# Kernel optimization log

Measured on AMD Instinct MI355X. Metric: run time of the kernel, lower is better.

Reference implementation:

```python
import jax, jax.numpy as jnp
import numpy as np
import math

D_MODEL = 2048
NUM_HEADS = 16
HEAD_DIM = D_MODEL // NUM_HEADS  # 128
B, S = 2, 2048


def setup_inputs() -> dict:
    key = jax.random.key(0)
    ks = jax.random.split(key, 11)
    s_in = 1.0 / math.sqrt(D_MODEL)
    return {
        "query": jax.random.normal(ks[0], (B, S, D_MODEL), dtype=jnp.float32),
        "key": jax.random.normal(ks[1], (B, S, D_MODEL), dtype=jnp.float32),
        "value": jax.random.normal(ks[2], (B, S, D_MODEL), dtype=jnp.float32),
        "Wq": jax.random.normal(ks[3], (D_MODEL, D_MODEL), dtype=jnp.float32) * s_in,
        "bq": jnp.zeros((D_MODEL,), dtype=jnp.float32),
        "Wk": jax.random.normal(ks[4], (D_MODEL, HEAD_DIM), dtype=jnp.float32) * s_in,
        "bk": jnp.zeros((HEAD_DIM,), dtype=jnp.float32),
        "Wv": jax.random.normal(ks[5], (D_MODEL, HEAD_DIM), dtype=jnp.float32) * s_in,
        "bv": jnp.zeros((HEAD_DIM,), dtype=jnp.float32),
        "Wo": jax.random.normal(ks[6], (D_MODEL, D_MODEL), dtype=jnp.float32) * s_in,
        "bo": jnp.zeros((D_MODEL,), dtype=jnp.float32),
    }


def reference(query, key, value, Wq, bq, Wk, bk, Wv, bv, Wo, bo):
    b, s, d_model = query.shape
    h, d = NUM_HEADS, HEAD_DIM
    # Projections: Q has h heads, K/V have a single shared head (MQA)
    Q = (query @ Wq + bq).reshape(b, s, h, d).transpose(0, 2, 1, 3)  # [b,h,s,d]
    K = key @ Wk + bk      # [b,s,d]
    V = value @ Wv + bv    # [b,s,d]
    scale = 1.0 / math.sqrt(d)
    # broadcast single K head over all h query heads
    scores = jnp.einsum('bhqd,bkd->bhqk', Q, K) * scale  # [b,h,s,s]
    weights = jax.nn.softmax(scores, axis=-1)
    attn = jnp.einsum('bhqk,bkd->bhqd', weights, V)      # [b,h,s,d]
    attn = attn.transpose(0, 2, 1, 3).reshape(b, s, d_model)
    return attn @ Wo + bo
```

## Files before the change

kernel.cpp:

```cpp
#include <hip/hip_runtime.h>


typedef unsigned short u16;
typedef __attribute__((ext_vector_type(8))) short bf16x8;
typedef __attribute__((ext_vector_type(4))) short bf16x4;
typedef __attribute__((ext_vector_type(4))) float f32x4;

#define D_MODEL 2048
#define SEQ     2048
#define NH      16
#define HD      128
#define BK      32

__device__ __forceinline__ u16 f2bf(float f){
  union { float f; unsigned u; } v; v.f = f;
  unsigned r = (v.u + 0x7FFFu + ((v.u >> 16) & 1u)) >> 16;
  return (u16)r;
}

#if __has_builtin(__builtin_amdgcn_cvt_pk_bf16_f32)
__device__ __forceinline__ unsigned pack2bf(float a, float b){
  auto v = __builtin_amdgcn_cvt_pk_bf16_f32(a, b);
  unsigned u; __builtin_memcpy(&u, &v, 4); return u;
}
#else
__device__ __forceinline__ unsigned pack2bf(float a, float b){
  return (unsigned)f2bf(a) | ((unsigned)f2bf(b) << 16);
}
#endif

__device__ __forceinline__ void gll16(const void* g, void* l){
  __builtin_amdgcn_global_load_lds(
      (const __attribute__((address_space(1))) void*)g,
      (__attribute__((address_space(3))) void*)l, 16, 0, 0);
}

__global__ __launch_bounds__(256) void convert3_kernel(
    const float4* __restrict__ a, const float4* __restrict__ b, const float4* __restrict__ c,
    ushort4* __restrict__ oa, ushort4* __restrict__ ob, ushort4* __restrict__ oc){
  int i = blockIdx.x*256 + threadIdx.x;
  float4 va = a[i], vb = b[i], vc = c[i];
  ushort4 ra, rb, rc;
  ra.x=f2bf(va.x); ra.y=f2bf(va.y); ra.z=f2bf(va.z); ra.w=f2bf(va.w);
  rb.x=f2bf(vb.x); rb.y=f2bf(vb.y); rb.z=f2bf(vb.z); rb.w=f2bf(vb.w);
  rc.x=f2bf(vc.x); rc.y=f2bf(vc.y); rc.z=f2bf(vc.z); rc.w=f2bf(vc.w);
  oa[i]=ra; ob[i]=rb; oc[i]=rc;
}

__global__ __launch_bounds__(256) void transpose_all(
    const float* __restrict__ Wq, const float* __restrict__ Wo,
    const float* __restrict__ Wk, const float* __restrict__ Wv,
    u16* __restrict__ WqT, u16* __restrict__ WoT,
    u16* __restrict__ WkT, u16* __restrict__ WvT){
  __shared__ float tt[32][33];
  int id = blockIdx.x;
  const float* in; u16* outp; int C, bx, by;
  if (id < 4096)      { in=Wq; outp=WqT; C=2048; bx=id&63;        by=id>>6; }
  else if (id < 8192) { id-=4096; in=Wo; outp=WoT; C=2048; bx=id&63; by=id>>6; }
  else if (id < 8448) { id-=8192; in=Wk; outp=WkT; C=128;  bx=id&3;  by=id>>2; }
  else                { id-=8448; in=Wv; outp=WvT; C=128;  bx=id&3;  by=id>>2; }
  const int R = 2048;
  int c0 = bx*32, r0 = by*32;
  int tx = threadIdx.x & 31, ty = threadIdx.x >> 5;
  #pragma unroll
  for (int k=0;k<4;k++) tt[ty+k*8][tx] = in[(size_t)(r0+ty+k*8)*C + c0+tx];
  __syncthreads();
  #pragma unroll
  for (int k=0;k<4;k++) outp[(size_t)(c0+ty+k*8)*R + r0+tx] = f2bf(tt[tx][ty+k*8]);
}

__device__ __forceinline__ void gemm_core_db(
    const u16* __restrict__ A, const u16* __restrict__ BT,
    int lda, int ldb, int m0, int n0, int kbeg, int kend,
    u16* As, u16* Bs, f32x4 acc[4][4])
{
  const int t = threadIdx.x;
  const int w = t >> 6, l = t & 63;
  const int wr = w >> 1, wc = w & 1;
  const int c16 = l & 15, q = l >> 4;
  const int srow = l >> 2;
  const int sc   = ((l & 3) ^ ((l >> 3) & 3)) * 8;

  int aoff[4], boff[4];
  #pragma unroll
  for (int mt=0;mt<4;mt++){
    int row = wr*64 + mt*16 + c16;
    aoff[mt] = row*BK + ((q ^ ((row>>1)&3))*8);
  }
  #pragma unroll
  for (int nt=0;nt<4;nt++){
    int row = wc*64 + nt*16 + c16;
    boff[nt] = row*BK + ((q ^ ((row>>1)&3))*8);
  }

  auto issue = [&](int k0, int buf){
    u16* Ad = As + buf*4096;
    u16* Bd = Bs + buf*4096;
    #pragma unroll
    for (int half=0; half<2; half++){
      int r = half*64 + w*16 + srow;
      gll16(A  + (size_t)(m0+r)*lda + k0 + sc, Ad + (half*64 + w*16)*BK);
      gll16(BT + (size_t)(n0+r)*ldb + k0 + sc, Bd + (half*64 + w*16)*BK);
    }
  };

  const int n = (kend - kbeg) / BK;
  issue(kbeg, 0);
  for (int i = 0; i < n; i++){
    __syncthreads();
    if (i+1 < n) issue(kbeg + (i+1)*BK, (i+1)&1);
    const u16* Ab = As + (i&1)*4096;
    const u16* Bb = Bs + (i&1)*4096;
    bf16x8 af[4], bfr[4];
    #pragma unroll
    for (int mt=0;mt<4;mt++) af[mt]  = *(const bf16x8*)(Ab + aoff[mt]);
    #pragma unroll
    for (int nt=0;nt<4;nt++) bfr[nt] = *(const bf16x8*)(Bb + boff[nt]);
    #pragma unroll
    for (int mt=0;mt<4;mt++)
      #pragma unroll
      for (int nt=0;nt<4;nt++)
        acc[mt][nt] = __builtin_amdgcn_mfma_f32_16x16x32_bf16(af[mt], bfr[nt], acc[mt][nt], 0,0,0);
  }
}

__global__ __launch_bounds__(256) void proj_kernel(
    const u16* __restrict__ qb, const u16* __restrict__ kb, const u16* __restrict__ vb,
    const u16* __restrict__ WqT, const u16* __restrict__ WkT, const u16* __restrict__ WvT,
    const float* __restrict__ bq, u16* __restrict__ Qp, float* __restrict__ part)
{
  __shared__ u16 As[2*4096], Bs[2*4096];
  f32x4 acc[4][4];
  f32x4 z = {0.f,0.f,0.f,0.f};
  #pragma unroll
  for (int i=0;i<4;i++) for (int j=0;j<4;j++) acc[i][j] = z;
  const int t = threadIdx.x, w = t>>6, l = t&63, wr = w>>1, wc = w&1, c16 = l&15, q = l>>4;
  int id = blockIdx.x;
  if (id < 512){
    int m0 = (id & 31)*128, n0 = (id >> 5)*128;
    gemm_core_db(qb, WqT, 2048, 2048, m0, n0, 0, 2048, As, Bs, acc);
    #pragma unroll
    for (int mt=0;mt<4;mt++)
      #pragma unroll
      for (int nt=0;nt<4;nt++){
        int col = n0 + wc*64 + nt*16 + c16;
        float bv = bq[col];
        #pragma unroll
        for (int r=0;r<4;r++){
          int row = m0 + wr*64 + mt*16 + q*4 + r;
          Qp[(size_t)row*D_MODEL + col] = f2bf(acc[mt][nt][r] + bv);
        }
      }
  } else {
    int kvid = id - 512;
    int zi = kvid & 3, nb = (kvid >> 2) & 1, mi = kvid >> 3;
    const u16* Am = nb ? vb  : kb;
    const u16* Bm = nb ? WvT : WkT;
    gemm_core_db(Am, Bm, 2048, 2048, mi*128, 0, zi*512, zi*512+512, As, Bs, acc);
    float* dst = part + (size_t)(zi*2 + nb)*524288;
    #pragma unroll
    for (int mt=0;mt<4;mt++)
      #pragma unroll
      for (int nt=0;nt<4;nt++){
        int col = wc*64 + nt*16 + c16;
        #pragma unroll
        for (int r=0;r<4;r++){
          int row = mi*128 + wr*64 + mt*16 + q*4 + r;
          dst[(size_t)row*128 + col] = acc[mt][nt][r];
        }
      }
  }
}

__global__ __launch_bounds__(256) void oproj_kernel(
    const u16* __restrict__ A, const u16* __restrict__ BT, const float* __restrict__ bias,
    float* __restrict__ C)
{
  __shared__ u16 As[2*4096], Bs[2*4096];
  f32x4 acc[4][4];
  f32x4 z = {0.f,0.f,0.f,0.f};
  #pragma unroll
  for (int i=0;i<4;i++) for (int j=0;j<4;j++) acc[i][j] = z;
  int m0 = blockIdx.x*128, n0 = blockIdx.y*128;
  gemm_core_db(A, BT, 2048, 2048, m0, n0, 0, 2048, As, Bs, acc);
  const int t = threadIdx.x, w = t>>6, l = t&63, wr = w>>1, wc = w&1, c16 = l&15, q = l>>4;
  #pragma unroll
  for (int mt=0;mt<4;mt++)
    #pragma unroll
    for (int nt=0;nt<4;nt++){
      int col = n0 + wc*64 + nt*16 + c16;
      float bv = bias[col];
      #pragma unroll
      for (int r=0;r<4;r++){
        int row = m0 + wr*64 + mt*16 + q*4 + r;
        C[(size_t)row*D_MODEL + col] = acc[mt][nt][r] + bv;
      }
    }
}

__global__ __launch_bounds__(256) void kv_reduce_kernel(
    const float* __restrict__ part, const float* __restrict__ bk, const float* __restrict__ bv,
    u16* __restrict__ Kp, u16* __restrict__ VpT){
  int idx = blockIdx.x*256 + threadIdx.x;
  int d = idx & 127, sg = idx >> 7;
  float ka = 0.f, va = 0.f;
  #pragma unroll
  for (int zi=0; zi<4; zi++){
    ka += part[(size_t)(zi*2+0)*524288 + idx];
    va += part[(size_t)(zi*2+1)*524288 + idx];
  }
  Kp[idx] = f2bf(ka + bk[d]);
  int b = sg >> 11, sl = sg & 2047;
  VpT[(size_t)b*262144 + (size_t)d*2048 + sl] = f2bf(va + bv[d]);
}

__global__ __launch_bounds__(256, 2) void attn_kernel(
    const u16* __restrict__ Qp, const u16* __restrict__ Kp,
    const u16* __restrict__ VpT, u16* __restrict__ attnb){
  __shared__ u16 lds[32768];
  u16* Ks = lds;
  u16* Vs = lds + 16384;
  const int t = threadIdx.x;
  const int w = t >> 6, l = t & 63;
  const int c16 = l & 15, q = l >> 4;

  const int qt = blockIdx.x;
  const int bh = blockIdx.y;
  const int b = bh >> 4, h = bh & 15;

  const u16* Qbase = Qp  + ((size_t)(b*SEQ + qt*128 + w*32))*D_MODEL + h*HD;
  const u16* Kbase = Kp  + (size_t)(b*SEQ)*HD;
  const u16* Vbase = VpT + (size_t)b*HD*SEQ;

  {
    u16* qtmp = lds + 16384 + w*4096;
    #pragma unroll
    for (int j=0;j<8;j++){
      int r = j*4 + (l >> 4);
      int g = (l & 15) ^ (r & 15);
      gll16(Qbase + (size_t)r*D_MODEL + g*8, qtmp + j*512);
    }
  }
  #pragma unroll
  for (int j=0;j<8;j++){
    int r = j*16 + w*4 + (l >> 4);
    int g = (l & 15) ^ (r & 15);
    gll16(Kbase + (size_t)r*HD + g*8, Ks + j*2048 + w*512);
  }
  __syncthreads();
  bf16x8 qf[2][4];
  #pragma unroll
  for (int qs=0;qs<2;qs++)
    #pragma unroll
    for (int kk=0;kk<4;kk++){
      int ch = kk*4 + q;
      qf[qs][kk] = *(const bf16x8*)(lds + 16384 + w*4096 + (qs*16 + c16)*128 + ((ch ^ c16) & 15)*8);
    }
  __syncthreads();

  f32x4 o[2][8];
  f32x4 z4 = {0.f,0.f,0.f,0.f};
  #pragma unroll
  for (int qs=0;qs<2;qs++) for (int dt=0;dt<8;dt++) o[qs][dt] = z4;
  float mrow[2] = {-1e30f, -1e30f};
  float lrow[2] = {0.f, 0.f};
  const float cs = 0.08838834764831845f * 1.4426950408889634f;

  for (int kt = 0; kt < 16; kt++){
    #pragma unroll
    for (int j=0;j<8;j++){
      int d = j*16 + w*4 + (l >> 4);
      int g = (l & 15) ^ (d & 15);
      gll16(Vbase + (size_t)d*SEQ + kt*128 + g*8, Vs + j*2048 + w*512);
    }

    f32x4 s[2][8];
    #pragma unroll
    for (int qs=0;qs<2;qs++) for (int kt8=0;kt8<8;kt8++) s[qs][kt8] = z4;
    #pragma unroll
    for (int kt8=0; kt8<8; kt8++){
      #pragma unroll
      for (int kk=0;kk<4;kk++){
        int ch = kk*4 + q;
        bf16x8 kf = *(const bf16x8*)(Ks + (kt8*16 + c16)*128 + ((ch ^ c16) & 15)*8);
        s[0][kt8] = __builtin_amdgcn_mfma_f32_16x16x32_bf16(kf, qf[0][kk], s[0][kt8], 0,0,0);
        s[1][kt8] = __builtin_amdgcn_mfma_f32_16x16x32_bf16(kf, qf[1][kk], s[1][kt8], 0,0,0);
      }
    }

    float alpha[2];
    #pragma unroll
    for (int qs=0; qs<2; qs++){
      float vmax = s[qs][0][0];
      #pragma unroll
      for (int kt8=0;kt8<8;kt8++)
        #pragma unroll
        for (int r=0;r<4;r++) vmax = fmaxf(vmax, s[qs][kt8][r]);
      vmax = fmaxf(vmax, __shfl_xor(vmax, 16));
      vmax = fmaxf(vmax, __shfl_xor(vmax, 32));
      float mold = mrow[qs];
      float mnew = fmaxf(mold, vmax);
      float a = exp2f((mold - mnew)*cs);
      float mc = mnew*cs;
      float rsum = 0.f;
      #pragma unroll
      for (int kt8=0;kt8<8;kt8++)
        #pragma unroll
        for (int r=0;r<4;r++){
          float p = exp2f(__builtin_fmaf(s[qs][kt8][r], cs, -mc));
          s[qs][kt8][r] = p; rsum += p;
        }
      rsum += __shfl_xor(rsum, 16);
      rsum += __shfl_xor(rsum, 32);
      lrow[qs] = lrow[qs]*a + rsum;
      mrow[qs] = mnew;
      alpha[qs] = a;
    }
    unsigned long long allone = __ballot(alpha[0] == 1.f && alpha[1] == 1.f);
    if (allone != ~0ull){
      #pragma unroll
      for (int qs=0;qs<2;qs++)
        #pragma unroll
        for (int dt=0;dt<8;dt++)
          #pragma unroll
          for (int r=0;r<4;r++) o[qs][dt][r] *= alpha[qs];
    }

    union { unsigned u[2]; bf16x4 v; } P[2][8];
    #pragma unroll
    for (int kt8=0;kt8<8;kt8++){
      P[0][kt8].u[0] = pack2bf(s[0][kt8][0], s[0][kt8][1]);
      P[0][kt8].u[1] = pack2bf(s[0][kt8][2], s[0][kt8][3]);
      P[1][kt8].u[0] = pack2bf(s[1][kt8][0], s[1][kt8][1]);
      P[1][kt8].u[1] = pack2bf(s[1][kt8][2], s[1][kt8][3]);
    }

    __syncthreads();

    if (kt < 15){
      #pragma unroll
      for (int j=0;j<8;j++){
        int r = j*16 + w*4 + (l >> 4);
        int g = (l & 15) ^ (r & 15);
        gll16(Kbase + (size_t)((kt+1)*128 + r)*HD + g*8, Ks + j*2048 + w*512);
      }
    }

    #pragma unroll
    for (int kt8=0; kt8<8; kt8++){
      int c4 = kt8*4 + q;
      #pragma unroll
      for (int dt=0; dt<8; dt++){
        int d = dt*16 + c16;
        int p8 = (c4 >> 1) ^ (d & 15);
        bf16x4 vf = *(const bf16x4*)(Vs + d*128 + p8*8 + (c4 & 1)*4);
        o[0][dt] = __builtin_amdgcn_mfma_f32_16x16x16bf16_1k(vf, P[0][kt8].v, o[0][dt], 0,0,0);
        o[1][dt] = __builtin_amdgcn_mfma_f32_16x16x16bf16_1k(vf, P[1][kt8].v, o[1][dt], 0,0,0);
      }
    }
    __syncthreads();
  }

  #pragma unroll
  for (int qs=0;qs<2;qs++){
    float inv = 1.f / lrow[qs];
    int qrow = qt*128 + w*32 + qs*16 + c16;
    u16* dst = attnb + ((size_t)(b*SEQ) + qrow)*D_MODEL + h*HD + q*4;
    #pragma unroll
    for (int dt=0;dt<8;dt++){
      ushort4 pk;
      pk.x = f2bf(o[qs][dt][0]*inv);
      pk.y = f2bf(o[qs][dt][1]*inv);
      pk.z = f2bf(o[qs][dt][2]*inv);
      pk.w = f2bf(o[qs][dt][3]*inv);
      *(ushort4*)(dst + dt*16) = pk;
    }
  }
}

extern "C" void kernel_launch(void* const* d_in, const int* in_sizes, int n_in,
                              void* d_out, int out_size, void* d_ws, size_t ws_size,
                              hipStream_t stream) {
  (void)in_sizes; (void)n_in; (void)out_size; (void)ws_size;
  const float* query = (const float*)d_in[0];
  const float* key   = (const float*)d_in[1];
  const float* value = (const float*)d_in[2];
  const float* Wq    = (const float*)d_in[3];
  const float* bq    = (const float*)d_in[4];
  const float* Wk    = (const float*)d_in[5];
  const float* bk    = (const float*)d_in[6];
  const float* Wv    = (const float*)d_in[7];
  const float* bv    = (const float*)d_in[8];
  const float* Wo    = (const float*)d_in[9];
  const float* bo    = (const float*)d_in[10];
  float* out = (float*)d_out;

  char* W = (char*)d_ws;
  u16*  qb     = (u16*) (W + 0);
  u16*  kb     = (u16*) (W + 16777216);
  u16*  vb     = (u16*) (W + 33554432);
  u16*  WqT    = (u16*) (W + 50331648);
  u16*  WoT    = (u16*) (W + 58720256);
  u16*  WkT    = (u16*) (W + 67108864);
  u16*  WvT    = (u16*) (W + 67633152);
  u16*  Qp     = (u16*) (W + 68157440);
  u16*  Kp     = (u16*) (W + 84934656);
  u16*  VpT    = (u16*) (W + 85983232);
  u16*  attnb  = (u16*) (W + 87031808);
  float* kvpart= (float*)(W + 103809024);

  convert3_kernel<<<8192, 256, 0, stream>>>(
      (const float4*)query, (const float4*)key, (const float4*)value,
      (ushort4*)qb, (ushort4*)kb, (ushort4*)vb);
  transpose_all<<<8704, 256, 0, stream>>>(Wq, Wo, Wk, Wv, WqT, WoT, WkT, WvT);
  proj_kernel<<<768, 256, 0, stream>>>(qb, kb, vb, WqT, WkT, WvT, bq, Qp, kvpart);
  kv_reduce_kernel<<<2048, 256, 0, stream>>>(kvpart, bk, bv, Kp, VpT);
  attn_kernel<<<dim3(16,32), 256, 0, stream>>>(Qp, Kp, VpT, attnb);
  oproj_kernel<<<dim3(32,16), 256, 0, stream>>>(attnb, WoT, bo, out);
}
```

Before: 416.8 us.

## Use 8 waves of 16 query rows each and 32-wide PV MFMA in attention

```diff
diff --git a/kernel.cpp b/kernel.cpp
--- a/kernel.cpp
+++ b/kernel.cpp
@@ -214,7 +214,7 @@
   VpT[(size_t)b*262144 + (size_t)d*2048 + sl] = f2bf(va + bv[d]);
 }
 
-__global__ __launch_bounds__(256, 2) void attn_kernel(
+__global__ __launch_bounds__(512, 4) void attn_kernel(
     const u16* __restrict__ Qp, const u16* __restrict__ Kp,
     const u16* __restrict__ VpT, u16* __restrict__ attnb){
   __shared__ u16 lds[32768];
@@ -228,153 +228,148 @@
   const int bh = blockIdx.y;
   const int b = bh >> 4, h = bh & 15;
 
-  const u16* Qbase = Qp  + ((size_t)(b*SEQ + qt*128 + w*32))*D_MODEL + h*HD;
+  const u16* Qbase = Qp  + ((size_t)(b*SEQ + qt*128 + w*16))*D_MODEL + h*HD;
   const u16* Kbase = Kp  + (size_t)(b*SEQ)*HD;
   const u16* Vbase = VpT + (size_t)b*HD*SEQ;
 
   {
-    u16* qtmp = lds + 16384 + w*4096;
-    #pragma unroll
-    for (int j=0;j<8;j++){
+    u16* qtmp = Vs + w*2048;
+    #pragma unroll
+    for (int j=0;j<4;j++){
       int r = j*4 + (l >> 4);
       int g = (l & 15) ^ (r & 15);
       gll16(Qbase + (size_t)r*D_MODEL + g*8, qtmp + j*512);
     }
   }
   #pragma unroll
-  for (int j=0;j<8;j++){
-    int r = j*16 + w*4 + (l >> 4);
+  for (int j=0;j<4;j++){
+    int r = j*32 + w*4 + (l >> 4);
     int g = (l & 15) ^ (r & 15);
-    gll16(Kbase + (size_t)r*HD + g*8, Ks + j*2048 + w*512);
+    gll16(Kbase + (size_t)r*HD + g*8, Ks + j*4096 + w*512);
   }
   __syncthreads();
-  bf16x8 qf[2][4];
-  #pragma unroll
-  for (int qs=0;qs<2;qs++)
-    #pragma unroll
-    for (int kk=0;kk<4;kk++){
-      int ch = kk*4 + q;
-      qf[qs][kk] = *(const bf16x8*)(lds + 16384 + w*4096 + (qs*16 + c16)*128 + ((ch ^ c16) & 15)*8);
-    }
+  bf16x8 qf[4];
+  #pragma unroll
+  for (int kk=0;kk<4;kk++){
+    int ch = kk*4 + q;
+    qf[kk] = *(const bf16x8*)(Vs + w*2048 + c16*128 + ((ch ^ c16) & 15)*8);
+  }
   __syncthreads();
 
-  f32x4 o[2][8];
+  f32x4 o[8];
   f32x4 z4 = {0.f,0.f,0.f,0.f};
   #pragma unroll
-  for (int qs=0;qs<2;qs++) for (int dt=0;dt<8;dt++) o[qs][dt] = z4;
-  float mrow[2] = {-1e30f, -1e30f};
-  float lrow[2] = {0.f, 0.f};
+  for (int dt=0;dt<8;dt++) o[dt] = z4;
+  float mrow = -1e30f, lrow = 0.f;
   const float cs = 0.08838834764831845f * 1.4426950408889634f;
 
   for (int kt = 0; kt < 16; kt++){
     #pragma unroll
-    for (int j=0;j<8;j++){
-      int d = j*16 + w*4 + (l >> 4);
+    for (int j=0;j<4;j++){
+      int d = j*32 + w*4 + (l >> 4);
       int g = (l & 15) ^ (d & 15);
-      gll16(Vbase + (size_t)d*SEQ + kt*128 + g*8, Vs + j*2048 + w*512);
-    }
-
-    f32x4 s[2][8];
-    #pragma unroll
-    for (int qs=0;qs<2;qs++) for (int kt8=0;kt8<8;kt8++) s[qs][kt8] = z4;
+      gll16(Vbase + (size_t)d*SEQ + kt*128 + g*8, Vs + j*4096 + w*512);
+    }
+
+    f32x4 s[8];
+    #pragma unroll
+    for (int kt8=0;kt8<8;kt8++) s[kt8] = z4;
+    __builtin_amdgcn_s_setprio(1);
     #pragma unroll
     for (int kt8=0; kt8<8; kt8++){
       #pragma unroll
       for (int kk=0;kk<4;kk++){
         int ch = kk*4 + q;
         bf16x8 kf = *(const bf16x8*)(Ks + (kt8*16 + c16)*128 + ((ch ^ c16) & 15)*8);
-        s[0][kt8] = __builtin_amdgcn_mfma_f32_16x16x32_bf16(kf, qf[0][kk], s[0][kt8], 0,0,0);
-        s[1][kt8] = __builtin_amdgcn_mfma_f32_16x16x32_bf16(kf, qf[1][kk], s[1][kt8], 0,0,0);
-      }
-    }
-
-    float alpha[2];
-    #pragma unroll
-    for (int qs=0; qs<2; qs++){
-      float vmax = s[qs][0][0];
-      #pragma unroll
-      for (int kt8=0;kt8<8;kt8++)
+        s[kt8] = __builtin_amdgcn_mfma_f32_16x16x32_bf16(kf, qf[kk], s[kt8], 0,0,0);
+      }
+    }
+    __builtin_amdgcn_s_setprio(0);
+
+    float x[8];
+    #pragma unroll
+    for (int kt8=0;kt8<8;kt8++)
+      x[kt8] = fmaxf(fmaxf(s[kt8][0],s[kt8][1]), fmaxf(s[kt8][2],s[kt8][3]));
+    float vmax = fmaxf(fmaxf(fmaxf(x[0],x[1]),fmaxf(x[2],x[3])),
+                       fmaxf(fmaxf(x[4],x[5]),fmaxf(x[6],x[7])));
+    vmax = fmaxf(vmax, __shfl_xor(vmax, 16));
+    vmax = fmaxf(vmax, __shfl_xor(vmax, 32));
+    float mnew = fmaxf(mrow, vmax);
+    float alpha = exp2f((mrow - mnew)*cs);
+    float mc = mnew*cs;
+    float rs[8];
+    #pragma unroll
+    for (int kt8=0;kt8<8;kt8++){
+      float p0 = exp2f(__builtin_fmaf(s[kt8][0], cs, -mc));
+      float p1 = exp2f(__builtin_fmaf(s[kt8][1], cs, -mc));
+      float p2 = exp2f(__builtin_fmaf(s[kt8][2], cs, -mc));
+      float p3 = exp2f(__builtin_fmaf(s[kt8][3], cs, -mc));
+      s[kt8][0]=p0; s[kt8][1]=p1; s[kt8][2]=p2; s[kt8][3]=p3;
+      rs[kt8] = (p0+p1)+(p2+p3);
+    }
+    float rsum = ((rs[0]+rs[1])+(rs[2]+rs[3])) + ((rs[4]+rs[5])+(rs[6]+rs[7]));
+    rsum += __shfl_xor(rsum, 16);
+    rsum += __shfl_xor(rsum, 32);
+    lrow = lrow*alpha + rsum;
+    mrow = mnew;
+
+    unsigned long long allone = __ballot(alpha == 1.f);
+    if (allone != ~0ull){
+      #pragma unroll
+      for (int dt=0;dt<8;dt++)
         #pragma unroll
-        for (int r=0;r<4;r++) vmax = fmaxf(vmax, s[qs][kt8][r]);
-      vmax = fmaxf(vmax, __shfl_xor(vmax, 16));
-      vmax = fmaxf(vmax, __shfl_xor(vmax, 32));
-      float mold = mrow[qs];
-      float mnew = fmaxf(mold, vmax);
-      float a = exp2f((mold - mnew)*cs);
-      float mc = mnew*cs;
-      float rsum = 0.f;
-      #pragma unroll
-      for (int kt8=0;kt8<8;kt8++)
-        #pragma unroll
-        for (int r=0;r<4;r++){
-          float p = exp2f(__builtin_fmaf(s[qs][kt8][r], cs, -mc));
-          s[qs][kt8][r] = p; rsum += p;
-        }
-      rsum += __shfl_xor(rsum, 16);
-      rsum += __shfl_xor(rsum, 32);
-      lrow[qs] = lrow[qs]*a + rsum;
-      mrow[qs] = mnew;
-      alpha[qs] = a;
-    }
-    unsigned long long allone = __ballot(alpha[0] == 1.f && alpha[1] == 1.f);
-    if (allone != ~0ull){
-      #pragma unroll
-      for (int qs=0;qs<2;qs++)
-        #pragma unroll
-        for (int dt=0;dt<8;dt++)
-          #pragma unroll
-          for (int r=0;r<4;r++) o[qs][dt][r] *= alpha[qs];
-    }
-
-    union { unsigned u[2]; bf16x4 v; } P[2][8];
-    #pragma unroll
-    for (int kt8=0;kt8<8;kt8++){
-      P[0][kt8].u[0] = pack2bf(s[0][kt8][0], s[0][kt8][1]);
-      P[0][kt8].u[1] = pack2bf(s[0][kt8][2], s[0][kt8][3]);
-      P[1][kt8].u[0] = pack2bf(s[1][kt8][0], s[1][kt8][1]);
-      P[1][kt8].u[1] = pack2bf(s[1][kt8][2], s[1][kt8][3]);
+        for (int r=0;r<4;r++) o[dt][r] *= alpha;
+    }
+
+    union PU { unsigned u[4]; bf16x8 v; } P32[4];
+    #pragma unroll
+    for (int kb=0;kb<4;kb++){
+      P32[kb].u[0] = pack2bf(s[2*kb][0],   s[2*kb][1]);
+      P32[kb].u[1] = pack2bf(s[2*kb][2],   s[2*kb][3]);
+      P32[kb].u[2] = pack2bf(s[2*kb+1][0], s[2*kb+1][1]);
+      P32[kb].u[3] = pack2bf(s[2*kb+1][2], s[2*kb+1][3]);
     }
 
     __syncthreads();
 
     if (kt < 15){
       #pragma unroll
-      for (int j=0;j<8;j++){
-        int r = j*16 + w*4 + (l >> 4);
+      for (int j=0;j<4;j++){
+        int r = j*32 + w*4 + (l >> 4);
         int g = (l & 15) ^ (r & 15);
-        gll16(Kbase + (size_t)((kt+1)*128 + r)*HD + g*8, Ks + j*2048 + w*512);
-      }
-    }
-
-    #pragma unroll
-    for (int kt8=0; kt8<8; kt8++){
-      int c4 = kt8*4 + q;
+        gll16(Kbase + (size_t)((kt+1)*128 + r)*HD + g*8, Ks + j*4096 + w*512);
+      }
+    }
+
+    __builtin_amdgcn_s_setprio(1);
+    #pragma unroll
+    for (int kb=0; kb<4; kb++){
+      int ca = 4*kb + (q>>1);
+      int cb = ca + 2;
       #pragma unroll
       for (int dt=0; dt<8; dt++){
         int d = dt*16 + c16;
-        int p8 = (c4 >> 1) ^ (d & 15);
-        bf16x4 vf = *(const bf16x4*)(Vs + d*128 + p8*8 + (c4 & 1)*4);
-        o[0][dt] = __builtin_amdgcn_mfma_f32_16x16x16bf16_1k(vf, P[0][kt8].v, o[0][dt], 0,0,0);
-        o[1][dt] = __builtin_amdgcn_mfma_f32_16x16x16bf16_1k(vf, P[1][kt8].v, o[1][dt], 0,0,0);
-      }
-    }
+        union VU { bf16x4 h[2]; bf16x8 v; } vf;
+        vf.h[0] = *(const bf16x4*)(Vs + d*128 + ((ca ^ c16) & 15)*8 + (q&1)*4);
+        vf.h[1] = *(const bf16x4*)(Vs + d*128 + ((cb ^ c16) & 15)*8 + (q&1)*4);
+        o[dt] = __builtin_amdgcn_mfma_f32_16x16x32_bf16(vf.v, P32[kb].v, o[dt], 0,0,0);
+      }
+    }
+    __builtin_amdgcn_s_setprio(0);
     __syncthreads();
   }
 
-  #pragma unroll
-  for (int qs=0;qs<2;qs++){
-    float inv = 1.f / lrow[qs];
-    int qrow = qt*128 + w*32 + qs*16 + c16;
-    u16* dst = attnb + ((size_t)(b*SEQ) + qrow)*D_MODEL + h*HD + q*4;
-    #pragma unroll
-    for (int dt=0;dt<8;dt++){
-      ushort4 pk;
-      pk.x = f2bf(o[qs][dt][0]*inv);
-      pk.y = f2bf(o[qs][dt][1]*inv);
-      pk.z = f2bf(o[qs][dt][2]*inv);
-      pk.w = f2bf(o[qs][dt][3]*inv);
-      *(ushort4*)(dst + dt*16) = pk;
-    }
+  float inv = 1.f / lrow;
+  int qrow = qt*128 + w*16 + c16;
+  u16* dst = attnb + ((size_t)(b*SEQ) + qrow)*D_MODEL + h*HD + q*4;
+  #pragma unroll
+  for (int dt=0;dt<8;dt++){
+    ushort4 pk;
+    pk.x = f2bf(o[dt][0]*inv);
+    pk.y = f2bf(o[dt][1]*inv);
+    pk.z = f2bf(o[dt][2]*inv);
+    pk.w = f2bf(o[dt][3]*inv);
+    *(ushort4*)(dst + dt*16) = pk;
   }
 }
 
@@ -415,6 +410,6 @@
   transpose_all<<<8704, 256, 0, stream>>>(Wq, Wo, Wk, Wv, WqT, WoT, WkT, WvT);
   proj_kernel<<<768, 256, 0, stream>>>(qb, kb, vb, WqT, WkT, WvT, bq, Qp, kvpart);
   kv_reduce_kernel<<<2048, 256, 0, stream>>>(kvpart, bk, bv, Kp, VpT);
-  attn_kernel<<<dim3(16,32), 256, 0, stream>>>(Qp, Kp, VpT, attnb);
+  attn_kernel<<<dim3(16,32), 512, 0, stream>>>(Qp, Kp, VpT, attnb);
   oproj_kernel<<<dim3(32,16), 256, 0, stream>>>(attnb, WoT, bo, out);
 }
```

New measurement: 432.4 us. 3.7% more time.
